# Performance work log

Hardware: AMD Instinct MI355X
Metric: run time of the kernel (lower is better)

Reference implementation:

```python
import jax, jax.numpy as jnp
import numpy as np

DIM = 1024
N = 8192


def setup_inputs() -> dict:
    key = jax.random.key(0)
    k_x, k_w, k_b = jax.random.split(key, 3)
    inputs = jax.random.normal(k_x, (N, DIM), dtype=jnp.float32)
    # nn.Bilinear(dimension, dimension, 1): weight shape (1, d, d), bias shape (1,)
    bound = 1.0 / np.sqrt(DIM)
    W = jax.random.uniform(k_w, (DIM, DIM), jnp.float32, -bound, bound)
    b = jax.random.uniform(k_b, (1,), jnp.float32, -bound, bound)
    return {"inputs": inputs, "W": W, "b": b}


def reference(inputs, W, b):
    # out[i, j] = inputs[i] @ W @ inputs[j] + b  ==  (X @ W) @ X^T + b
    # Algebraically identical to repeat+nn.Bilinear, without the N^2*d blowup.
    xw = inputs @ W              # (N, d)
    out = xw @ inputs.T + b[0]   # (N, N)
    return out
```

## Files before the change

### kernel.cpp

```cpp
#include <hip/hip_runtime.h>
#include <hip/hip_bf16.h>

typedef __bf16 bf16;
typedef __bf16 bf16x8 __attribute__((ext_vector_type(8)));
typedef __bf16 bf16x4 __attribute__((ext_vector_type(4)));
typedef float  f32x4  __attribute__((ext_vector_type(4)));

#define GLD_LDS(g, l)                                                        \
  __builtin_amdgcn_global_load_lds(                                          \
      (const __attribute__((address_space(1))) void*)(g),                    \
      (__attribute__((address_space(3))) void*)(l), 16, 0, 0)

#define SB()    __builtin_amdgcn_s_barrier()
#define WVM(n)  asm volatile("s_waitcnt vmcnt(" #n ")" ::: "memory")
#define PRIO1() __builtin_amdgcn_s_setprio(1)
#define PRIO0() __builtin_amdgcn_s_setprio(0)

template <int EPI, int NP>
__global__ __launch_bounds__(512, 2)
void gemm256(const bf16* __restrict__ A, const bf16* __restrict__ B,
             bf16* __restrict__ Cb, float* __restrict__ Cf,
             const float* __restrict__ bias_p, int M) {
  constexpr int KP = 1024;
  constexpr int NT = KP / 64;
  extern __shared__ bf16 lds[];
  const int tid  = threadIdx.x;
  const int lane = tid & 63, wave = tid >> 6;
  const int wm = wave >> 2, wn = wave & 3;
  const int fr = lane & 15, fq = lane >> 4;
  const int xm = (fr & 7) << 4;
  const int kx0 = (fq * 16) ^ xm;
  const int kx1 = (fq * 16 + 64) ^ xm;

  const int nwg = gridDim.x;
  const int bid = blockIdx.x;
  constexpr int gx = NP >> 8;
  const int nTiles = (M >> 8) * gx;
  const int rounds = nTiles / nwg;

  const int srow = wave * 8 + (lane >> 3);
  const int scol = ((lane & 7) ^ (lane >> 3)) * 8;

  bf16* ldsA = lds + wave * 512;
  bf16* ldsB = lds + 32768 + wave * 512;
  const char* ldsc = (const char*)lds;
  const char* Ab0 = ldsc + wm * 16384 + fr * 128 + kx0;
  const char* Ab1 = ldsc + wm * 16384 + fr * 128 + kx1;
  const char* Bb0 = ldsc + 65536 + wn * 8192 + fr * 128 + kx0;
  const char* Bb1 = ldsc + 65536 + wn * 8192 + fr * 128 + kx1;

  const float bias = (EPI == 1) ? bias_p[0] : 0.0f;

#define STG2(p0, p1, trel, base, off)                                        \
  do {                                                                       \
    GLD_LDS((p0) + (trel) * 64, (base) + (off));                             \
    GLD_LDS((p1) + (trel) * 64, (base) + (off) + 4096);                      \
  } while (0)

#define LDA4(mg, kk, p)                                                      \
  do {                                                                       \
    _Pragma("unroll") for (int m_ = 0; m_ < 4; ++m_)                         \
      af[m_][kk] = *(const bf16x8*)(Ab##kk + (p) * 32768 +                   \
                                    ((mg) * 4 + m_) * 2048);                 \
  } while (0)

#define LDB2(np, kk, p)                                                      \
  do {                                                                       \
    _Pragma("unroll") for (int n_ = 0; n_ < 2; ++n_)                         \
      bg[(np) * 2 + n_][kk] = *(const bf16x8*)(Bb##kk + (p) * 32768 +        \
                                               ((np) * 2 + n_) * 2048);      \
  } while (0)

#define MM(mg, np)                                                           \
  do {                                                                       \
    _Pragma("unroll") for (int kk_ = 0; kk_ < 2; ++kk_)                      \
      _Pragma("unroll") for (int m_ = 0; m_ < 4; ++m_)                       \
        _Pragma("unroll") for (int n_ = 0; n_ < 2; ++n_)                     \
          acc[(mg) * 4 + m_][(np) * 2 + n_] =                                \
              __builtin_amdgcn_mfma_f32_16x16x32_bf16(                       \
                  af[m_][kk_], bg[(np) * 2 + n_][kk_],                       \
                  acc[(mg) * 4 + m_][(np) * 2 + n_], 0, 0, 0);               \
  } while (0)

#define PHASE(RDS, STAGE, MMC, GATE)                                         \
  do { RDS; STAGE; SB(); PRIO1(); MMC; PRIO0(); GATE; SB(); } while (0)

#define RD1 do { LDB2(0,0,0); LDA4(0,0,0); LDB2(0,1,0); LDA4(0,1,0); } while(0)
#define RD2 do { LDB2(1,0,0); LDB2(1,1,0); } while(0)
#define RD3 do { LDA4(1,0,0); LDA4(1,1,0); } while(0)
#define RD5 do { LDB2(0,0,1); LDA4(0,0,1); LDB2(0,1,1); LDA4(0,1,1); } while(0)
#define RD6 do { LDB2(1,0,1); LDB2(1,1,1); } while(0)
#define RD7 do { LDA4(1,0,1); LDA4(1,1,1); } while(0)

  auto mapTile = [&](int rd, int& tr, int& tc) {
    if (NP == 8192 && nwg == 256 && (M >> 8) == 32) {
      const int xcd = bid & 7, pos = bid >> 3;
      tr = (rd >> 1) * 16 + (xcd >> 1) * 4 + (pos >> 3);
      tc = (rd & 1) * 16 + (xcd & 1) * 8 + (pos & 7);
    } else {
      const int li = rd * nwg + bid;
      const int swz = (li & 7) * (nTiles >> 3) + (li >> 3);
      tr = li < nTiles ? swz / gx : 0; tc = li < nTiles ? swz % gx : 0;
    }
  };

  int tr, tc;
  mapTile(0, tr, tc);
  int row0 = tr << 8, col0 = tc << 8;

  const bf16* a0 = A + (size_t)(row0 + srow) * KP + scol;
  const bf16* a1 = a0 + (size_t)64 * KP;
  const bf16* a2 = a0 + (size_t)128 * KP;
  const bf16* a3 = a0 + (size_t)192 * KP;
  const bf16* b0 = B + (size_t)(col0 + srow) * KP + scol;
  const bf16* b1 = b0 + (size_t)64 * KP;
  const bf16* b2 = b0 + (size_t)128 * KP;
  const bf16* b3 = b0 + (size_t)192 * KP;

  STG2(a0, a1, 0, ldsA, 0);
  STG2(a2, a3, 0, ldsA, 8192);
  STG2(b0, b1, 0, ldsB, 0);
  STG2(b2, b3, 0, ldsB, 8192);
  STG2(a0, a1, 1, ldsA, 16384);

  for (int rd = 0; rd < rounds; ++rd) {
    if (rd == 0) { WVM(2); } else { WVM(63); }
    SB();

    f32x4  acc[8][4] = {};
    bf16x8 af[4][2];
    bf16x8 bg[4][2];

#pragma unroll 1
    for (int it = 0; it < NT / 2 - 1; ++it) {
      PHASE(RD1, STG2(a2, a3, 1, ldsA, 24576), MM(0, 0), );
      PHASE(RD2, STG2(b0, b1, 1, ldsB, 16384), MM(0, 1), );
      PHASE(RD3, STG2(b2, b3, 1, ldsB, 24576), MM(1, 0), );
      PHASE(   , STG2(a0, a1, 2, ldsA, 0),     MM(1, 1), WVM(2));
      PHASE(RD5, STG2(a2, a3, 2, ldsA, 8192),  MM(0, 0), );
      PHASE(RD6, STG2(b0, b1, 2, ldsB, 0),     MM(0, 1), );
      PHASE(RD7, STG2(b2, b3, 2, ldsB, 8192),  MM(1, 0), );
      PHASE(   , STG2(a0, a1, 3, ldsA, 16384), MM(1, 1), WVM(2));
      a0 += 128; a1 += 128; a2 += 128; a3 += 128;
      b0 += 128; b1 += 128; b2 += 128; b3 += 128;
    }

    const bool hn = (rd + 1 < rounds);
    int ntr, ntc;
    mapTile(rd + 1, ntr, ntc);
    const int nrow0 = ntr << 8, ncol0 = ntc << 8;
    const bf16* na0 = A + (size_t)(nrow0 + srow) * KP + scol;
    const bf16* na1 = na0 + (size_t)64 * KP;
    const bf16* na2 = na0 + (size_t)128 * KP;
    const bf16* na3 = na0 + (size_t)192 * KP;
    const bf16* nb0 = B + (size_t)(ncol0 + srow) * KP + scol;
    const bf16* nb1 = nb0 + (size_t)64 * KP;
    const bf16* nb2 = nb0 + (size_t)128 * KP;
    const bf16* nb3 = nb0 + (size_t)192 * KP;

    PHASE(RD1, STG2(a2, a3, 1, ldsA, 24576), MM(0, 0), );
    PHASE(RD2, STG2(b0, b1, 1, ldsB, 16384), MM(0, 1), );
    PHASE(RD3, STG2(b2, b3, 1, ldsB, 24576), MM(1, 0), );
    PHASE(   , if (hn) { STG2(na0, na1, 0, ldsA, 0); },    MM(1, 1),
           if (hn) { WVM(2); } else { WVM(0); });
    PHASE(RD5, if (hn) { STG2(na2, na3, 0, ldsA, 8192); }, MM(0, 0), );
    PHASE(RD6, if (hn) { STG2(nb0, nb1, 0, ldsB, 0); },    MM(0, 1), );
    PHASE(RD7, if (hn) { STG2(nb2, nb3, 0, ldsB, 8192); }, MM(1, 0), );
    PHASE(   , if (hn) { STG2(na0, na1, 1, ldsA, 16384); }, MM(1, 1),
           if (hn) { WVM(2); } else { WVM(0); });

#pragma unroll
    for (int m = 0; m < 8; ++m) {
#pragma unroll
      for (int n = 0; n < 4; ++n) {
        const int r = row0 + wm * 128 + m * 16 + fq * 4;
        const int c = col0 + wn * 64 + n * 16 + fr;
#pragma unroll
        for (int j = 0; j < 4; ++j) {
          if (EPI == 1)
            Cf[(size_t)(r + j) * NP + c] = acc[m][n][j] + bias;
          else
            Cb[(size_t)(r + j) * NP + c] = (bf16)acc[m][n][j];
        }
      }
    }

    a0 = na0; a1 = na1; a2 = na2; a3 = na3;
    b0 = nb0; b1 = nb1; b2 = nb2; b3 = nb3;
    row0 = nrow0; col0 = ncol0;
  }
#undef STG2
#undef LDA4
#undef LDB2
#undef MM
#undef PHASE
#undef RD1
#undef RD2
#undef RD3
#undef RD5
#undef RD6
#undef RD7
}

__global__ void cvt_f32_bf16(const float* __restrict__ in, bf16* __restrict__ out,
                             int n4) {
  int i = blockIdx.x * blockDim.x + threadIdx.x;
  if (i >= n4) return;
  const float4 v = ((const float4*)in)[i];
  bf16x4 o;
  o[0] = (bf16)v.x; o[1] = (bf16)v.y; o[2] = (bf16)v.z; o[3] = (bf16)v.w;
  ((bf16x4*)out)[i] = o;
}

__global__ void transpose_cvt_w(const float* __restrict__ W, bf16* __restrict__ Wt) {
  __shared__ float s[32][33];
  const int tx = threadIdx.x & 31;
  const int ty = threadIdx.x >> 5;
  const int n0 = blockIdx.x * 32;
  const int k0 = blockIdx.y * 32;
#pragma unroll
  for (int p = 0; p < 4; ++p)
    s[ty + p * 8][tx] = W[(size_t)(k0 + ty + p * 8) * 1024 + n0 + tx];
  __syncthreads();
#pragma unroll
  for (int p = 0; p < 4; ++p)
    Wt[(size_t)(n0 + ty + p * 8) * 1024 + k0 + tx] = (bf16)s[tx][ty + p * 8];
}

extern "C" void kernel_launch(void* const* d_in, const int* in_sizes, int n_in,
                              void* d_out, int out_size, void* d_ws, size_t ws_size,
                              hipStream_t stream) {
  const float* X = (const float*)d_in[0];
  const float* W = (const float*)d_in[1];
  const float* b = (const float*)d_in[2];
  float* out = (float*)d_out;

  const int Nn = 8192, D = 1024;
  char* ws = (char*)d_ws;
  bf16* Xb  = (bf16*)(ws);
  bf16* XWb = (bf16*)(ws + (size_t)16 * 1024 * 1024);
  bf16* Wt  = (bf16*)(ws + (size_t)32 * 1024 * 1024);

  cvt_f32_bf16<<<(Nn * D / 4 + 255) / 256, 256, 0, stream>>>(X, Xb, Nn * D / 4);
  transpose_cvt_w<<<dim3(D / 32, D / 32), 256, 0, stream>>>(W, Wt);
  gemm256<0, 1024><<<128, 512, 131072, stream>>>(Xb, Wt, XWb, nullptr, nullptr,
                                                 Nn);
  gemm256<1, 8192><<<256, 512, 131072, stream>>>(XWb, Xb, nullptr, out, b, Nn);
}
```

Measured before the change: 189.8 us.

## Use 128x128 tile GEMM for X@W and merge prep kernels

Adds a new 128x128-tile GEMM kernel with 512 blocks and 64KB LDS for the first X@W product, replacing the 256-tile kernel that launched only 128 blocks and left many compute units idle. The two preprocessing kernels (X conversion and W transpose-convert) are fused into a single launch to save one kernel launch. The smaller tile lowers data reuse per block but aims to fill the GPU better for the 8192x1024 output.

```diff
diff --git a/kernel.cpp b/kernel.cpp
--- a/kernel.cpp
+++ b/kernel.cpp
@@ -15,6 +15,8 @@
 #define WVM(n)  asm volatile("s_waitcnt vmcnt(" #n ")" ::: "memory")
 #define PRIO1() __builtin_amdgcn_s_setprio(1)
 #define PRIO0() __builtin_amdgcn_s_setprio(0)
+
+extern __shared__ char lds[];
 
 template <int EPI, int NP>
 __global__ __launch_bounds__(512, 2)
@@ -23,7 +25,7 @@
              const float* __restrict__ bias_p, int M) {
   constexpr int KP = 1024;
   constexpr int NT = KP / 64;
-  extern __shared__ bf16 lds[];
+  bf16* ldsh = (bf16*)lds;
   const int tid  = threadIdx.x;
   const int lane = tid & 63, wave = tid >> 6;
   const int wm = wave >> 2, wn = wave & 3;
@@ -41,9 +43,9 @@
   const int srow = wave * 8 + (lane >> 3);
   const int scol = ((lane & 7) ^ (lane >> 3)) * 8;
 
-  bf16* ldsA = lds + wave * 512;
-  bf16* ldsB = lds + 32768 + wave * 512;
-  const char* ldsc = (const char*)lds;
+  bf16* ldsA = ldsh + wave * 512;
+  bf16* ldsB = ldsh + 32768 + wave * 512;
+  const char* ldsc = (const char*)ldsh;
   const char* Ab0 = ldsc + wm * 16384 + fr * 128 + kx0;
   const char* Ab1 = ldsc + wm * 16384 + fr * 128 + kx1;
   const char* Bb0 = ldsc + 65536 + wn * 8192 + fr * 128 + kx0;
@@ -202,29 +204,137 @@
 #undef RD7
 }
 
-__global__ void cvt_f32_bf16(const float* __restrict__ in, bf16* __restrict__ out,
-                             int n4) {
-  int i = blockIdx.x * blockDim.x + threadIdx.x;
-  if (i >= n4) return;
-  const float4 v = ((const float4*)in)[i];
-  bf16x4 o;
-  o[0] = (bf16)v.x; o[1] = (bf16)v.y; o[2] = (bf16)v.z; o[3] = (bf16)v.w;
-  ((bf16x4*)out)[i] = o;
+template <int EPI, int NP>
+__global__ __launch_bounds__(512, 4)
+void gemm128k(const bf16* __restrict__ A, const bf16* __restrict__ B,
+              bf16* __restrict__ Cb, float* __restrict__ Cf,
+              const float* __restrict__ bias_p, int M) {
+  constexpr int KP = 1024;
+  constexpr int NT = KP / 64;
+  const int tid  = threadIdx.x;
+  const int lane = tid & 63, wave = tid >> 6;
+  const int wm = wave >> 1, wn = wave & 1;
+  const int fr = lane & 15, fq = lane >> 4;
+  const int laneb = (fr >> 1) * 128 + ((((fr & 1) * 4 + fq) ^ ((fr >> 1) & 7)) << 4);
+
+  const int bid = blockIdx.x;
+  constexpr int gx = NP >> 7;
+  const int nTiles = (M >> 7) * gx;
+  int tr, tc;
+  {
+    const int swz = (bid & 7) * (nTiles >> 3) + (bid >> 3);
+    tr = swz / gx; tc = swz % gx;
+  }
+  const int row0 = tr << 7, col0 = tc << 7;
+
+  const int gsw  = (tid & 7) ^ ((tid >> 3) & 7);
+  const int srow = 2 * (tid >> 3) + (gsw >> 2);
+  const int chnk = gsw & 3;
+  const bf16* Agl = A + (size_t)(row0 + srow) * KP + chnk * 8;
+  const bf16* Bgl = B + (size_t)(col0 + srow) * KP + chnk * 8;
+
+#define STG1(gp, base_off, t, kk)                                            \
+  GLD_LDS((gp) + (size_t)(t) * 64 + (kk) * 32,                               \
+          lds + (base_off) + ((t) & 1) * 16384 + (kk) * 8192 + wave * 1024)
+
+  const char* Ab = lds + wm * 2048 + laneb;
+  const char* Bb = lds + 32768 + wn * 4096 + laneb;
+
+  f32x4  acc[2][4] = {};
+  bf16x8 af[2], bg[4];
+
+#define LDA(kk, p)                                                           \
+  do {                                                                       \
+    _Pragma("unroll") for (int m_ = 0; m_ < 2; ++m_)                         \
+      af[m_] = *(const bf16x8*)(Ab + (p) * 16384 + (kk) * 8192 + m_ * 1024); \
+  } while (0)
+
+#define LDBH(np, kk, p)                                                      \
+  do {                                                                       \
+    _Pragma("unroll") for (int n_ = 0; n_ < 2; ++n_)                         \
+      bg[(np) * 2 + n_] = *(const bf16x8*)(Bb + (p) * 16384 + (kk) * 8192 +  \
+                                           ((np) * 2 + n_) * 1024);          \
+  } while (0)
+
+#define MM(np)                                                               \
+  do {                                                                       \
+    _Pragma("unroll") for (int m_ = 0; m_ < 2; ++m_)                         \
+      _Pragma("unroll") for (int n_ = 0; n_ < 2; ++n_)                       \
+        acc[m_][(np) * 2 + n_] = __builtin_amdgcn_mfma_f32_16x16x32_bf16(    \
+            af[m_], bg[(np) * 2 + n_], acc[m_][(np) * 2 + n_], 0, 0, 0);     \
+  } while (0)
+
+  STG1(Agl, 0, 0, 0); STG1(Bgl, 32768, 0, 0);
+  STG1(Agl, 0, 0, 1); STG1(Bgl, 32768, 0, 1);
+  WVM(2); SB();
+
+  for (int T = 0; T < NT; ++T) {
+    const int p = T & 1;
+    const bool st = (T + 1 < NT);
+    LDA(0, p); LDBH(0, 0, p);
+    if (st) STG1(Agl, 0, T + 1, 0);
+    PRIO1(); MM(0); PRIO0();
+    LDBH(1, 0, p);
+    if (st) STG1(Bgl, 32768, T + 1, 0);
+    PRIO1(); MM(1); PRIO0();
+    if (st) { WVM(2); } else { WVM(0); }
+    SB();
+    LDA(1, p); LDBH(0, 1, p);
+    if (st) STG1(Agl, 0, T + 1, 1);
+    PRIO1(); MM(0); PRIO0();
+    LDBH(1, 1, p);
+    if (st) STG1(Bgl, 32768, T + 1, 1);
+    PRIO1(); MM(1); PRIO0();
+    if (st) { WVM(2); } else { WVM(0); }
+    SB();
+  }
+
+  const float bias = (EPI == 1) ? bias_p[0] : 0.0f;
+#pragma unroll
+  for (int m = 0; m < 2; ++m) {
+#pragma unroll
+    for (int n = 0; n < 4; ++n) {
+      const int r = row0 + wm * 32 + m * 16 + fq * 4;
+      const int c = col0 + wn * 64 + n * 16 + fr;
+#pragma unroll
+      for (int j = 0; j < 4; ++j) {
+        if (EPI == 1)
+          Cf[(size_t)(r + j) * NP + c] = acc[m][n][j] + bias;
+        else
+          Cb[(size_t)(r + j) * NP + c] = (bf16)acc[m][n][j];
+      }
+    }
+  }
+#undef STG1
+#undef LDA
+#undef LDBH
+#undef MM
 }
 
-__global__ void transpose_cvt_w(const float* __restrict__ W, bf16* __restrict__ Wt) {
+__global__ void prep(const float* __restrict__ X, bf16* __restrict__ Xb,
+                     const float* __restrict__ W, bf16* __restrict__ Wt) {
   __shared__ float s[32][33];
-  const int tx = threadIdx.x & 31;
-  const int ty = threadIdx.x >> 5;
-  const int n0 = blockIdx.x * 32;
-  const int k0 = blockIdx.y * 32;
-#pragma unroll
-  for (int p = 0; p < 4; ++p)
-    s[ty + p * 8][tx] = W[(size_t)(k0 + ty + p * 8) * 1024 + n0 + tx];
-  __syncthreads();
-#pragma unroll
-  for (int p = 0; p < 4; ++p)
-    Wt[(size_t)(n0 + ty + p * 8) * 1024 + k0 + tx] = (bf16)s[tx][ty + p * 8];
+  const int bid = blockIdx.x;
+  if (bid < 8192) {
+    const int i = bid * 256 + threadIdx.x;
+    const float4 v = ((const float4*)X)[i];
+    bf16x4 o;
+    o[0] = (bf16)v.x; o[1] = (bf16)v.y; o[2] = (bf16)v.z; o[3] = (bf16)v.w;
+    ((bf16x4*)Xb)[i] = o;
+  } else {
+    const int b2 = bid - 8192;
+    const int tx = threadIdx.x & 31;
+    const int ty = threadIdx.x >> 5;
+    const int n0 = (b2 & 31) * 32;
+    const int k0 = (b2 >> 5) * 32;
+#pragma unroll
+    for (int p = 0; p < 4; ++p)
+      s[ty + p * 8][tx] = W[(size_t)(k0 + ty + p * 8) * 1024 + n0 + tx];
+    __syncthreads();
+#pragma unroll
+    for (int p = 0; p < 4; ++p)
+      Wt[(size_t)(n0 + ty + p * 8) * 1024 + k0 + tx] = (bf16)s[tx][ty + p * 8];
+  }
 }
 
 extern "C" void kernel_launch(void* const* d_in, const int* in_sizes, int n_in,
@@ -235,15 +345,14 @@
   const float* b = (const float*)d_in[2];
   float* out = (float*)d_out;
 
-  const int Nn = 8192, D = 1024;
+  const int Nn = 8192;
   char* ws = (char*)d_ws;
   bf16* Xb  = (bf16*)(ws);
   bf16* XWb = (bf16*)(ws + (size_t)16 * 1024 * 1024);
   bf16* Wt  = (bf16*)(ws + (size_t)32 * 1024 * 1024);
 
-  cvt_f32_bf16<<<(Nn * D / 4 + 255) / 256, 256, 0, stream>>>(X, Xb, Nn * D / 4);
-  transpose_cvt_w<<<dim3(D / 32, D / 32), 256, 0, stream>>>(W, Wt);
-  gemm256<0, 1024><<<128, 512, 131072, stream>>>(Xb, Wt, XWb, nullptr, nullptr,
+  prep<<<9216, 256, 0, stream>>>(X, Xb, W, Wt);
+  gemm128k<0, 1024><<<512, 512, 65536, stream>>>(Xb, Wt, XWb, nullptr, nullptr,
                                                  Nn);
   gemm256<1, 8192><<<256, 512, 131072, stream>>>(XWb, Xb, nullptr, out, b, Nn);
 }
```

Measured after the change: 182.2 us. -4.0%, faster.
